# Optimization experiments

Measured on AMD Instinct MI355X. Metric: run time of the kernel, lower is better.

## Reference

```python
import jax, jax.numpy as jnp
import numpy as np

WIN = 9
PAD = WIN // 2
LOSS_WEIGHT = 1.0


def _box_sum(x):
    # x: [B,1,H,W]; 9x9 box-filter sum via conv2d with a ones kernel (SAME padding)
    k = jnp.ones((1, 1, WIN, WIN), dtype=x.dtype)
    return jax.lax.conv_general_dilated(
        x, k, window_strides=(1, 1), padding=[(PAD, PAD), (PAD, PAD)],
        dimension_numbers=('NCHW', 'OIHW', 'NCHW'))


def _ncc_map(I, J):
    I2, J2, IJ = I * I, J * J, I * J
    I_sum = _box_sum(I)
    J_sum = _box_sum(J)
    I2_sum = _box_sum(I2)
    J2_sum = _box_sum(J2)
    IJ_sum = _box_sum(IJ)
    n = float(WIN * WIN)
    u_I = I_sum / n
    u_J = J_sum / n
    cross = IJ_sum - u_J * I_sum - u_I * J_sum + u_I * u_J * n
    I_var = I2_sum - 2.0 * u_I * I_sum + u_I * u_I * n
    J_var = J2_sum - 2.0 * u_J * J_sum + u_J * u_J * n
    cc = cross * cross / (I_var * J_var + 1e-5)
    return 1.0 - cc


def setup_inputs() -> dict:
    key = jax.random.key(0)
    k1, k2, k3 = jax.random.split(key, 3)
    shape = (32, 1, 512, 512)
    return {
        'img1': jax.random.uniform(k1, shape, dtype=jnp.float32),
        'img2': jax.random.uniform(k2, shape, dtype=jnp.float32),
        'fusion_img': jax.random.uniform(k3, shape, dtype=jnp.float32),
    }


def reference(img1, img2, fusion_img):
    combined = (_ncc_map(img1, fusion_img) + _ncc_map(img2, fusion_img)) / 2.0
    return jnp.mean(combined) * LOSS_WEIGHT
```

## Files before the change

kernel.cpp:

```cpp
#include <hip/hip_runtime.h>

#define BATCH 32
#define H 512
#define W 512
#define PADR 4
#define WIN 9
#define SEG 16
#define COLS 4
#define NT 128
#define NSTEP (SEG + WIN - 1)
#define SCALE (0.5f / 8388608.0f)

typedef float v4f __attribute__((ext_vector_type(4)));

__global__ __launch_bounds__(NT, 1) void ncc_loss_kernel(
    const float* __restrict__ g1, const float* __restrict__ g2,
    const float* __restrict__ gf, float* __restrict__ out)
{
    const int t  = threadIdx.x;
    const int x0 = t * COLS;
    const int y0 = blockIdx.y * SEG;
    const int b  = blockIdx.z;
    const size_t base = (size_t)b * (size_t)(H * W);
    const int voff = x0 * 4;

    __shared__ __align__(16) float Vl[8][520];
    if (t < 64) {
        const int gp  = t & 7;
        const int q   = t >> 3;
        const int idx = (gp < 4) ? gp : (512 + gp);
        Vl[q][idx] = 0.0f;
    }

    v4f buf[2][3];
    auto load_row = [&](int step, int par) {
        const int yr  = y0 - PADR + step;
        const int rec = ((unsigned)yr < (unsigned)H) ? (W * 4) : 0;
        const int yc  = yr < 0 ? 0 : (yr >= H ? H - 1 : yr);
        const size_t roff = base + (size_t)yc * W;
        __amdgpu_buffer_rsrc_t r1 = __builtin_amdgcn_make_buffer_rsrc(
            (void*)(g1 + roff), (short)0, rec, 0x00020000);
        __amdgpu_buffer_rsrc_t r2 = __builtin_amdgcn_make_buffer_rsrc(
            (void*)(g2 + roff), (short)0, rec, 0x00020000);
        __amdgpu_buffer_rsrc_t rf = __builtin_amdgcn_make_buffer_rsrc(
            (void*)(gf + roff), (short)0, rec, 0x00020000);
        buf[par][0] = __builtin_bit_cast(v4f,
            __builtin_amdgcn_raw_buffer_load_b128(r1, voff, 0, 0));
        buf[par][1] = __builtin_bit_cast(v4f,
            __builtin_amdgcn_raw_buffer_load_b128(r2, voff, 0, 0));
        buf[par][2] = __builtin_bit_cast(v4f,
            __builtin_amdgcn_raw_buffer_load_b128(rf, voff, 0, 0));
    };

    float ring[3][WIN][COLS];
#pragma unroll
    for (int im = 0; im < 3; ++im)
#pragma unroll
        for (int i = 0; i < WIN; ++i)
#pragma unroll
            for (int c = 0; c < COLS; ++c) ring[im][i][c] = 0.f;

    float V[8][COLS];
#pragma unroll
    for (int q = 0; q < 8; ++q)
#pragma unroll
        for (int c = 0; c < COLS; ++c) V[q][c] = 0.f;

    float lsum = 0.f;
    const float inv_n = 1.0f / 81.0f;

    load_row(0, 0);

#pragma unroll
    for (int s = 0; s < NSTEP; ++s) {
        if (s + 1 < NSTEP) load_row(s + 1, (s + 1) & 1);

        const v4f A = buf[s & 1][0];
        const v4f C = buf[s & 1][1];
        const v4f F = buf[s & 1][2];
        const int ph = s % WIN;

#pragma unroll
        for (int c = 0; c < COLS; ++c) {
            const float n1 = A[c], n2 = C[c], nf = F[c];
            const float o1 = ring[0][ph][c], o2 = ring[1][ph][c],
                        of = ring[2][ph][c];
            V[0][c] += n1 - o1;
            V[1][c] += n2 - o2;
            V[2][c] += nf - of;
            V[3][c] = fmaf(n1, n1, fmaf(-o1, o1, V[3][c]));
            V[4][c] = fmaf(n2, n2, fmaf(-o2, o2, V[4][c]));
            V[5][c] = fmaf(nf, nf, fmaf(-of, of, V[5][c]));
            V[6][c] = fmaf(n1, nf, fmaf(-o1, of, V[6][c]));
            V[7][c] = fmaf(n2, nf, fmaf(-o2, of, V[7][c]));
            ring[0][ph][c] = n1; ring[1][ph][c] = n2; ring[2][ph][c] = nf;
        }

        if (s >= WIN - 1) {
            if (s > WIN - 1) __syncthreads();

            float Tq[8];
#pragma unroll
            for (int q = 0; q < 8; ++q) {
                const float p1 = V[q][0];
                const float p2 = p1 + V[q][1];
                const float p3 = p2 + V[q][2];
                const float tt = p3 + V[q][3];
                Tq[q] = tt;
                v4f v; v.x = p1; v.y = p2; v.z = p3; v.w = tt;
                *(v4f*)&Vl[q][4 + 4 * t] = v;
            }
            __syncthreads();

            float S[8][COLS];
#pragma unroll
            for (int q = 0; q < 8; ++q) {
                const v4f Lp = *(const v4f*)&Vl[q][4 * t];
                const v4f Rp = *(const v4f*)&Vl[q][4 * t + 8];
                const float lT  = Lp.w;
                const float TT  = Tq[q];
                S[q][0] = (lT         + TT) + Rp.x;
                S[q][1] = ((lT - Lp.x) + TT) + Rp.y;
                S[q][2] = ((lT - Lp.y) + TT) + Rp.z;
                S[q][3] = ((lT - Lp.z) + TT) + Rp.w;
            }

#pragma unroll
            for (int c = 0; c < COLS; ++c) {
                const float sA = S[0][c], sC = S[1][c], sF = S[2][c];
                const float u1 = sA * inv_n;
                const float u2 = sC * inv_n;
                const float uf = sF * inv_n;
                const float cross1 = fmaf(-sA, uf, S[6][c]);
                const float var1   = fmaf(-sA, u1, S[3][c]);
                const float varf   = fmaf(-sF, uf, S[5][c]);
                const float cross2 = fmaf(-sC, uf, S[7][c]);
                const float var2   = fmaf(-sC, u2, S[4][c]);
                const float d1 = fmaf(var1, varf, 1e-5f);
                const float d2 = fmaf(var2, varf, 1e-5f);
                const float inv = __builtin_amdgcn_rcpf(d1 * d2);
                float num = cross1 * cross1 * d2;
                num = fmaf(cross2 * cross2, d1, num);
                lsum += fmaf(-num, inv, 2.0f);
            }
        }
    }

#pragma unroll
    for (int offd = 32; offd > 0; offd >>= 1)
        lsum += __shfl_down(lsum, offd);
    __shared__ float wsum[2];
    const int lane = t & 63;
    const int wid  = t >> 6;
    if (lane == 0) wsum[wid] = lsum;
    __syncthreads();
    if (t == 0) atomicAdd(out, (wsum[0] + wsum[1]) * SCALE);
}

extern "C" void kernel_launch(void* const* d_in, const int* in_sizes, int n_in,
                              void* d_out, int out_size, void* d_ws, size_t ws_size,
                              hipStream_t stream) {
    const float* img1 = (const float*)d_in[0];
    const float* img2 = (const float*)d_in[1];
    const float* fimg = (const float*)d_in[2];
    float* out = (float*)d_out;

    hipMemsetAsync(out, 0, sizeof(float), stream);

    dim3 grid(1, H / SEG, BATCH);
    ncc_loss_kernel<<<grid, dim3(NT), 0, stream>>>(img1, img2, fimg, out);
}
```

Measured before the change: 133.1 us.

## Replace LDS neighbor exchange with DPP wave shifts and deepen row prefetch

Horizontal neighbor partial sums are now exchanged with DPP wave_shr/wave_shl lane moves instead of writing all partials to shared memory. Only the seam between the two wavefronts goes through a small double-buffered LDS array, which removes one barrier per output row. Row loads are now issued two steps ahead instead of one, so more memory latency is hidden. This adds DPP ops and per-lane selects at the seam, and relies on the zero fill at the wave edges (bound_ctrl) to supply the image-border padding.

```diff
diff --git a/kernel.cpp b/kernel.cpp
--- a/kernel.cpp
+++ b/kernel.cpp
@@ -13,6 +13,16 @@
 
 typedef float v4f __attribute__((ext_vector_type(4)));
 
+
+__device__ __forceinline__ float from_left(float v) {
+    return __builtin_bit_cast(float, __builtin_amdgcn_update_dpp(
+        0, __builtin_bit_cast(int, v), 0x138, 0xF, 0xF, true));
+}
+__device__ __forceinline__ float from_right(float v) {
+    return __builtin_bit_cast(float, __builtin_amdgcn_update_dpp(
+        0, __builtin_bit_cast(int, v), 0x130, 0xF, 0xF, true));
+}
+
 __global__ __launch_bounds__(NT, 1) void ncc_loss_kernel(
     const float* __restrict__ g1, const float* __restrict__ g2,
     const float* __restrict__ gf, float* __restrict__ out)
@@ -24,17 +34,10 @@
     const size_t base = (size_t)b * (size_t)(H * W);
     const int voff = x0 * 4;
 
-    __shared__ __align__(16) float Vl[8][520];
-    if (t < 64) {
-        const int gp  = t & 7;
-        const int q   = t >> 3;
-        const int idx = (gp < 4) ? gp : (512 + gp);
-        Vl[q][idx] = 0.0f;
-    }
+    __shared__ v4f seamL[2][8], seamR[2][8];
 
-    v4f buf[2][3];
-    auto load_row = [&](int step, int par) {
-        const int yr  = y0 - PADR + step;
+    v4f nA[3], nB[3];
+    auto issue3 = [&](int yr, v4f* dst) {
         const int rec = ((unsigned)yr < (unsigned)H) ? (W * 4) : 0;
         const int yc  = yr < 0 ? 0 : (yr >= H ? H - 1 : yr);
         const size_t roff = base + (size_t)yc * W;
@@ -44,11 +47,11 @@
             (void*)(g2 + roff), (short)0, rec, 0x00020000);
         __amdgpu_buffer_rsrc_t rf = __builtin_amdgcn_make_buffer_rsrc(
             (void*)(gf + roff), (short)0, rec, 0x00020000);
-        buf[par][0] = __builtin_bit_cast(v4f,
+        dst[0] = __builtin_bit_cast(v4f,
             __builtin_amdgcn_raw_buffer_load_b128(r1, voff, 0, 0));
-        buf[par][1] = __builtin_bit_cast(v4f,
+        dst[1] = __builtin_bit_cast(v4f,
             __builtin_amdgcn_raw_buffer_load_b128(r2, voff, 0, 0));
-        buf[par][2] = __builtin_bit_cast(v4f,
+        dst[2] = __builtin_bit_cast(v4f,
             __builtin_amdgcn_raw_buffer_load_b128(rf, voff, 0, 0));
     };
 
@@ -69,20 +72,17 @@
     float lsum = 0.f;
     const float inv_n = 1.0f / 81.0f;
 
-    load_row(0, 0);
+    issue3(y0 - PADR + 0, nA);
+    issue3(y0 - PADR + 1, nB);
 
 #pragma unroll
     for (int s = 0; s < NSTEP; ++s) {
-        if (s + 1 < NSTEP) load_row(s + 1, (s + 1) & 1);
-
-        const v4f A = buf[s & 1][0];
-        const v4f C = buf[s & 1][1];
-        const v4f F = buf[s & 1][2];
+        v4f* nb = (s & 1) ? nB : nA;
         const int ph = s % WIN;
 
 #pragma unroll
         for (int c = 0; c < COLS; ++c) {
-            const float n1 = A[c], n2 = C[c], nf = F[c];
+            const float n1 = nb[0][c], n2 = nb[1][c], nf = nb[2][c];
             const float o1 = ring[0][ph][c], o2 = ring[1][ph][c],
                         of = ring[2][ph][c];
             V[0][c] += n1 - o1;
@@ -96,33 +96,51 @@
             ring[0][ph][c] = n1; ring[1][ph][c] = n2; ring[2][ph][c] = nf;
         }
 
+        if (s + 2 < NSTEP) issue3(y0 - PADR + s + 2, nb);
         if (s >= WIN - 1) {
-            if (s > WIN - 1) __syncthreads();
+            const int par = s & 1;
 
-            float Tq[8];
+            float P[8][4];
 #pragma unroll
             for (int q = 0; q < 8; ++q) {
                 const float p1 = V[q][0];
                 const float p2 = p1 + V[q][1];
                 const float p3 = p2 + V[q][2];
-                const float tt = p3 + V[q][3];
-                Tq[q] = tt;
-                v4f v; v.x = p1; v.y = p2; v.z = p3; v.w = tt;
-                *(v4f*)&Vl[q][4 + 4 * t] = v;
+                const float T  = p3 + V[q][3];
+                P[q][0] = p1; P[q][1] = p2; P[q][2] = p3; P[q][3] = T;
+                if (t == 63) {
+                    v4f v; v.x = T; v.y = T - p1; v.z = T - p2; v.w = T - p3;
+                    seamL[par][q] = v;
+                }
+                if (t == 64) {
+                    v4f v; v.x = p1; v.y = p2; v.z = p3; v.w = T;
+                    seamR[par][q] = v;
+                }
             }
             __syncthreads();
 
-            float S[8][COLS];
+            float S[8][4];
 #pragma unroll
             for (int q = 0; q < 8; ++q) {
-                const v4f Lp = *(const v4f*)&Vl[q][4 * t];
-                const v4f Rp = *(const v4f*)&Vl[q][4 * t + 8];
-                const float lT  = Lp.w;
-                const float TT  = Tq[q];
-                S[q][0] = (lT         + TT) + Rp.x;
-                S[q][1] = ((lT - Lp.x) + TT) + Rp.y;
-                S[q][2] = ((lT - Lp.y) + TT) + Rp.z;
-                S[q][3] = ((lT - Lp.z) + TT) + Rp.w;
+                const float T  = P[q][3];
+                const float a0 = T;
+                const float a1 = T - P[q][0];
+                const float a2 = T - P[q][1];
+                const float a3 = T - P[q][2];
+                float l0 = from_left(a0), l1 = from_left(a1),
+                      l2 = from_left(a2), l3 = from_left(a3);
+                float r0 = from_right(P[q][0]), r1 = from_right(P[q][1]),
+                      r2 = from_right(P[q][2]), r3 = from_right(P[q][3]);
+                const v4f sl = seamL[par][q];
+                const v4f sr = seamR[par][q];
+                l0 = (t == 64) ? sl.x : l0;  l1 = (t == 64) ? sl.y : l1;
+                l2 = (t == 64) ? sl.z : l2;  l3 = (t == 64) ? sl.w : l3;
+                r0 = (t == 63) ? sr.x : r0;  r1 = (t == 63) ? sr.y : r1;
+                r2 = (t == 63) ? sr.z : r2;  r3 = (t == 63) ? sr.w : r3;
+                S[q][0] = (l0 + T) + r0;
+                S[q][1] = (l1 + T) + r1;
+                S[q][2] = (l2 + T) + r2;
+                S[q][3] = (l3 + T) + r3;
             }
 
 #pragma unroll
```

Result: slower. 171.1 us (+28.5%).
